# Performance work log

Measured on AMD Instinct MI355X. Metric: run time of the kernel, lower is better.

Reference implementation:

```python
import jax, jax.numpy as jnp
import numpy as np

# ---- dims (match init_kwargs) ----
IMG = 128; PATCH = 16; GRID = IMG // PATCH; L = GRID * GRID  # 64 patches
D = 256            # embed_dim
EXP = 2; DIN = D * EXP          # d_inner = 512
DH = 64; H = DIN // DH          # 8 heads
G = 1; N = 64                   # n_groups, d_state
DCONV = 4
DEPTH = 2
NCLS = 1000
BATCH = 16
DINPROJ = 2 * DIN + 2 * G * N + H   # z | xBC | dt
CDIM = DIN + 2 * G * N              # conv channels
EPS = 1e-6

def _snake_indices():
    g = np.arange(L).reshape(GRID, GRID)
    g[1::2] = g[1::2, ::-1]
    return jnp.asarray(g.reshape(-1))

SNAKE = _snake_indices()

def rmsnorm(x, w):
    return x * jax.lax.rsqrt(jnp.mean(x * x, axis=-1, keepdims=True) + EPS) * w

def causal_depthwise_conv(x, w, b):
    # x: (B,L,C), w: (C,K) depthwise causal conv, then SiLU
    xp = jnp.pad(x, ((0, 0), (DCONV - 1, 0), (0, 0)))
    y = sum(xp[:, k:k + x.shape[1], :] * w[:, k] for k in range(DCONV))
    return jax.nn.silu(y + b)

def mamba_block(x, Win, cw, cb, dtb, Alog, Dp, gn, Wout):
    # Mamba-2/3 style selective scan block. x: (B,L,D)
    Bsz, Lx, _ = x.shape
    zxbcdt = x @ Win                                   # (B,L,DINPROJ)
    z   = zxbcdt[..., :DIN]
    xBC = zxbcdt[..., DIN:DIN + CDIM]
    dt  = jax.nn.softplus(zxbcdt[..., DIN + CDIM:] + dtb)   # (B,L,H)
    xBC = causal_depthwise_conv(xBC, cw, cb)
    xs = xBC[..., :DIN].reshape(Bsz, Lx, H, DH)
    Bm = xBC[..., DIN:DIN + G * N].reshape(Bsz, Lx, G, N)
    Cm = xBC[..., DIN + G * N:].reshape(Bsz, Lx, G, N)
    Bh = jnp.repeat(Bm, H // G, axis=2)                # (B,L,H,N)
    Ch = jnp.repeat(Cm, H // G, axis=2)
    decay = jnp.exp(dt * (-jnp.exp(Alog)))             # (B,L,H) in (0,1)
    dBx = jnp.einsum('blh,blhp,blhn->blhpn', dt, xs, Bh)
    def step(h, inp):
        d, u = inp
        h = d[..., None, None] * h + u
        return h, h
    _, hs = jax.lax.scan(step, jnp.zeros((Bsz, H, DH, N), x.dtype),
                         (jnp.moveaxis(decay, 1, 0), jnp.moveaxis(dBx, 1, 0)))
    hs = jnp.moveaxis(hs, 0, 1)                        # (B,L,H,DH,N)
    y = jnp.einsum('blhpn,blhn->blhp', hs, Ch) + Dp[None, None, :, None] * xs
    y = y.reshape(Bsz, Lx, DIN)
    y = rmsnorm(y * jax.nn.silu(z), gn)                # gated RMSNorm
    return y @ Wout                                    # (B,L,D)

def setup_inputs() -> dict:
    key = jax.random.key(0)
    ks = jax.random.split(key, 24)
    s_in = 1.0 / np.sqrt(D); s_out = 1.0 / np.sqrt(DIN)
    def blk(k):
        kk = jax.random.split(k, 8)
        return dict(
            Win=jax.random.normal(kk[0], (DEPTH, D, DINPROJ)) * s_in,
            cw=jax.random.normal(kk[1], (DEPTH, CDIM, DCONV)) * 0.3,
            cb=jnp.zeros((DEPTH, CDIM)),
            dtb=jax.random.normal(kk[2], (DEPTH, H)) * 0.1,
            Alog=jnp.log(jax.random.uniform(kk[3], (DEPTH, H), minval=1.0, maxval=16.0)),
            Dp=jnp.ones((DEPTH, H)),
            gn=jnp.ones((DEPTH, DIN)),
            Wout=jax.random.normal(kk[4], (DEPTH, DIN, D)) * s_out)
    f = blk(ks[0]); b = blk(ks[1])
    inp = {
        'x': jax.random.normal(ks[2], (BATCH, 3, IMG, IMG), dtype=jnp.float32),
        'patch_w': jax.random.normal(ks[3], (D, 3 * PATCH * PATCH)) * (1.0 / np.sqrt(3 * PATCH * PATCH)),
        'patch_b': jnp.zeros((D,)),
        'pos_embed': jax.random.normal(ks[4], (1, L, D)) * 0.02,
        'norms_w': jnp.ones((DEPTH, D)),
        'final_w': jnp.ones((D,)),
        'head_w': jax.random.normal(ks[5], (D, NCLS)) * (1.0 / np.sqrt(D)),
        'head_b': jnp.zeros((NCLS,)),
    }
    for nm, v in f.items():
        inp[nm + '_f'] = v
    for nm, v in b.items():
        inp[nm + '_b'] = v
    return inp

def reference(x, patch_w, patch_b, pos_embed, norms_w, final_w, head_w, head_b,
              Win_f, cw_f, cb_f, dtb_f, Alog_f, Dp_f, gn_f, Wout_f,
              Win_b, cw_b, cb_b, dtb_b, Alog_b, Dp_b, gn_b, Wout_b):
    Bsz = x.shape[0]
    # patch embed == Conv2d(kernel=stride=PATCH)
    p = x.reshape(Bsz, 3, GRID, PATCH, GRID, PATCH).transpose(0, 2, 4, 1, 3, 5)
    p = p.reshape(Bsz, L, 3 * PATCH * PATCH)
    t = p @ patch_w.T + patch_b                        # (B,L,D)
    t = t + pos_embed[0]
    t = t[:, SNAKE, :]                                 # snake scan order
    for i in range(DEPTH):
        nx = rmsnorm(t, norms_w[i])
        of = mamba_block(nx, Win_f[i], cw_f[i], cb_f[i], dtb_f[i], Alog_f[i], Dp_f[i], gn_f[i], Wout_f[i])
        ob = mamba_block(nx[:, ::-1, :], Win_b[i], cw_b[i], cb_b[i], dtb_b[i], Alog_b[i], Dp_b[i], gn_b[i], Wout_b[i])[:, ::-1, :]
        t = t + 0.5 * (of + ob)                        # drop_path_rate=0 -> identity
    t = rmsnorm(t, final_w)
    t = t.mean(axis=1)
    return t @ head_w + head_b
```

## Files before the change

### kernel.cpp

```cpp
#include <hip/hip_runtime.h>
#include <hip/hip_bf16.h>
#include <math.h>

#define IMG 128
#define PATCH 16
#define L 64
#define D 256
#define DIN 512
#define DH 64
#define H 8
#define NSTATE 64
#define DCONV 4
#define DEPTH 2
#define NCLS 1000
#define BATCH 16
#define DINPROJ 1160
#define CDIM 640
#define EPS 1e-6f

typedef __attribute__((ext_vector_type(8))) short short8;
typedef __attribute__((ext_vector_type(4))) float f32x4;
typedef __attribute__((ext_vector_type(4))) unsigned short us4;
typedef unsigned short ushort_t;

__device__ __forceinline__ int snake_tok(int s){
    int r = s >> 3, c = s & 7;
    return (r & 1) ? (r * 8 + (7 - c)) : (r * 8 + c);
}
__device__ __forceinline__ float silu_f(float x){ return x / (1.f + expf(-x)); }
__device__ __forceinline__ float softplus_f(float x){ return x > 20.f ? x : log1pf(expf(x)); }
__device__ __forceinline__ ushort_t f2b(float f){
    __hip_bfloat16 h = __float2bfloat16(f);
    return *(ushort_t*)&h;
}

__global__ __launch_bounds__(256) void wconv_patch_k(
    const float* __restrict__ Win0, const float* __restrict__ Win1,
    const float* __restrict__ Wout0, const float* __restrict__ Wout1,
    ushort_t* __restrict__ wbuf,
    const float* __restrict__ x, const float* __restrict__ PW,
    float* __restrict__ part)
{
    __shared__ float sm[32][33];
    __shared__ __align__(16) ushort_t As[2][64][40];
    __shared__ __align__(16) ushort_t Bs[2][64][40];
    const int zall = blockIdx.z;
    if (zall < 8){
        int z = zall;
        int R, C; const float* src; ushort_t* dst;
        if (z < 4){
            int layer = z >> 1, dir = z & 1;
            src = (dir ? Win1 : Win0) + (size_t)layer * D * DINPROJ;
            dst = wbuf + (size_t)z * 296960;
            R = D; C = DINPROJ;
        } else {
            int zz = z - 4, layer = zz >> 1, dir = zz & 1;
            src = (dir ? Wout1 : Wout0) + (size_t)layer * DIN * D;
            dst = wbuf + 1187840 + (size_t)zz * 131072;
            R = DIN; C = D;
        }
        int ctiles = (C + 31) >> 5, rtiles = R >> 5;
        if (blockIdx.x >= ctiles || blockIdx.y >= rtiles) return;
        int c0 = blockIdx.x * 32, r0 = blockIdx.y * 32;
        int tx = threadIdx.x & 31, ty = threadIdx.x >> 5;
        #pragma unroll
        for (int k = 0; k < 4; ++k){
            int r = r0 + ty + 8 * k, c = c0 + tx;
            sm[ty + 8 * k][tx] = (c < C) ? src[(size_t)r * C + c] : 0.f;
        }
        __syncthreads();
        #pragma unroll
        for (int k = 0; k < 4; ++k){
            int dr = c0 + ty + 8 * k, dc = r0 + tx;
            if (dr < C) dst[(size_t)dr * R + dc] = f2b(sm[tx][ty + 8 * k]);
        }
        return;
    }
    if (blockIdx.x >= 4) return;
    const int t = threadIdx.x;
    const int n0 = blockIdx.x * 64;
    const int b  = blockIdx.y;
    const int split = zall - 8;
    const int kbase = split * 96;
    const int lrow = t >> 2, lc8 = (t & 3) * 8;
    const int tok = snake_tok(lrow), gy = tok >> 3, gx = tok & 7;
    const float* xb = x + (size_t)b * 3 * IMG * IMG;
    const int wave = t >> 6, lane = t & 63;
    const int wm = (wave >> 1) * 32, wn = (wave & 1) * 32;
    const int fro = lane & 15, fk = (lane >> 4) * 8;

    f32x4 acc[2][2];
    #pragma unroll
    for (int i = 0; i < 2; ++i)
        #pragma unroll
        for (int j = 0; j < 2; ++j) acc[i][j] = (f32x4){0.f,0.f,0.f,0.f};

    short8 areg, breg;
    auto gload = [&](int kk){
        int k = kk + lc8;
        int c = k >> 8, rem = k & 255, py = rem >> 4, px = rem & 15;
        const float* srcA = xb + ((size_t)c * IMG + gy * PATCH + py) * IMG + gx * PATCH + px;
        float4 a0 = *(const float4*)(srcA);
        float4 a1 = *(const float4*)(srcA + 4);
        ushort_t ta[8] = {f2b(a0.x),f2b(a0.y),f2b(a0.z),f2b(a0.w),
                          f2b(a1.x),f2b(a1.y),f2b(a1.z),f2b(a1.w)};
        areg = *(short8*)ta;
        const float* srcB = PW + (size_t)(n0 + lrow) * 768 + kk + lc8;
        float4 b0 = *(const float4*)(srcB);
        float4 b1 = *(const float4*)(srcB + 4);
        ushort_t tb[8] = {f2b(b0.x),f2b(b0.y),f2b(b0.z),f2b(b0.w),
                          f2b(b1.x),f2b(b1.y),f2b(b1.z),f2b(b1.w)};
        breg = *(short8*)tb;
    };
    auto sstore = [&](int buf){
        *(short8*)&As[buf][lrow][lc8] = areg;
        *(short8*)&Bs[buf][lrow][lc8] = breg;
    };

    const int nk = 3;
    gload(kbase); sstore(0);
    __syncthreads();
    for (int kt = 0; kt < nk; ++kt){
        const int buf = kt & 1;
        if (kt + 1 < nk) gload(kbase + (kt + 1) * 32);
        short8 af[2], bfr[2];
        af[0]  = *(const short8*)&As[buf][wm + fro][fk];
        af[1]  = *(const short8*)&As[buf][wm + 16 + fro][fk];
        bfr[0] = *(const short8*)&Bs[buf][wn + fro][fk];
        bfr[1] = *(const short8*)&Bs[buf][wn + 16 + fro][fk];
        #pragma unroll
        for (int i = 0; i < 2; ++i)
            #pragma unroll
            for (int j = 0; j < 2; ++j)
                acc[i][j] = __builtin_amdgcn_mfma_f32_16x16x32_bf16(af[i], bfr[j], acc[i][j], 0, 0, 0);
        if (kt + 1 < nk) sstore(buf ^ 1);
        __syncthreads();
    }
    float* Cp = part + (size_t)split * (BATCH * L * D);
    #pragma unroll
    for (int i = 0; i < 2; ++i){
        #pragma unroll
        for (int j = 0; j < 2; ++j){
            int col = n0 + wn + j * 16 + (lane & 15);
            #pragma unroll
            for (int r = 0; r < 4; ++r){
                int srow = wm + i * 16 + (lane >> 4) * 4 + r;
                Cp[(size_t)(b * 64 + srow) * D + col] = acc[i][j][r];
            }
        }
    }
}

__global__ void patch_red_k(const float* __restrict__ part, const float* __restrict__ pb,
                            const float* __restrict__ pos, float* __restrict__ t){
    int i = blockIdx.x * 256 + threadIdx.x;
    int d = i & (D - 1), s = (i >> 8) & (L - 1);
    float v = 0.f;
    #pragma unroll
    for (int r = 0; r < 8; ++r) v += part[i + r * (BATCH * L * D)];
    t[i] = v + pb[d] + pos[snake_tok(s) * D + d];
}

__global__ __launch_bounds__(256) void gemm_in_k(
    const float* __restrict__ T, const float* __restrict__ nw,
    const ushort_t* __restrict__ B0, const ushort_t* __restrict__ B1,
    const float* __restrict__ cw0, const float* __restrict__ cw1,
    const float* __restrict__ cb0, const float* __restrict__ cb1,
    const float* __restrict__ dtb0, const float* __restrict__ dtb1,
    const float* __restrict__ Al0, const float* __restrict__ Al1,
    float* __restrict__ zb0, float* __restrict__ zb1,
    float* __restrict__ xy0, float* __restrict__ xy1,
    float* __restrict__ bc0, float* __restrict__ bc1,
    float* __restrict__ dts0, float* __restrict__ dts1,
    float* __restrict__ cums0, float* __restrict__ cums1)
{
    __shared__ __align__(16) ushort_t As[64][264];
    __shared__ __align__(16) ushort_t Bs[2][64][40];
    __shared__ float Ctile[64][68];
    const int dir = blockIdx.z;
    const ushort_t* __restrict__ Bw = dir ? B1 : B0;
    const int t = threadIdx.x;
    const int m0 = blockIdx.y * 64, n0 = blockIdx.x * 64;
    const int b = blockIdx.y;
    const int arow = t >> 2;
    const int wave = t >> 6, lane = t & 63;
    const int wm = (wave >> 1) * 32, wn = (wave & 1) * 32;
    const int fro = lane & 15, fk = (lane >> 4) * 8;

    {
        const float* src = T + (size_t)(m0 + arow) * D;
        float ss = 0.f;
        #pragma unroll
        for (int i = 0; i < 16; ++i){
            int c = (t & 3) * 4 + i * 16;
            float4 v = *(const float4*)(src + c);
            ss += v.x*v.x + v.y*v.y + v.z*v.z + v.w*v.w;
        }
        ss += __shfl_xor(ss, 1);
        ss += __shfl_xor(ss, 2);
        float sc = rsqrtf(ss * (1.f / (float)D) + EPS);
        #pragma unroll
        for (int i = 0; i < 16; ++i){
            int c = (t & 3) * 4 + i * 16;
            float4 v = *(const float4*)(src + c);
            float4 w = *(const float4*)(nw + c);
            us4 o = {f2b(v.x*sc*w.x), f2b(v.y*sc*w.y), f2b(v.z*sc*w.z), f2b(v.w*sc*w.w)};
            *(us4*)&As[arow][c] = o;
        }
    }
    const int lrow = t >> 2, lc8 = (t & 3) * 8;
    float4 breg;
    auto gloadB = [&](int kk){
        int gn = n0 + lrow;
        if (gn < DINPROJ) breg = *(const float4*)(Bw + (size_t)gn * D + kk + lc8);
        else breg = make_float4(0.f,0.f,0.f,0.f);
    };
    auto sstoreB = [&](int buf){ *(float4*)&Bs[buf][lrow][lc8] = breg; };

    f32x4 acc[2][2];
    #pragma unroll
    for (int i = 0; i < 2; ++i)
        #pragma unroll
        for (int j = 0; j < 2; ++j) acc[i][j] = (f32x4){0.f,0.f,0.f,0.f};

    gloadB(0); sstoreB(0);
    __syncthreads();
    const int nk = D / 32;
    for (int kt = 0; kt < nk; ++kt){
        const int buf = kt & 1;
        if (kt + 1 < nk) gloadB((kt + 1) * 32);
        short8 af[2], bfr[2];
        af[0]  = *(const short8*)&As[wm + fro][kt * 32 + fk];
        af[1]  = *(const short8*)&As[wm + 16 + fro][kt * 32 + fk];
        bfr[0] = *(const short8*)&Bs[buf][wn + fro][fk];
        bfr[1] = *(const short8*)&Bs[buf][wn + 16 + fro][fk];
        #pragma unroll
        for (int i = 0; i < 2; ++i)
            #pragma unroll
            for (int j = 0; j < 2; ++j)
                acc[i][j] = __builtin_amdgcn_mfma_f32_16x16x32_bf16(af[i], bfr[j], acc[i][j], 0, 0, 0);
        if (kt + 1 < nk) sstoreB(buf ^ 1);
        __syncthreads();
    }

    if (n0 < DIN){
        float* zb = dir ? zb1 : zb0;
        #pragma unroll
        for (int i = 0; i < 2; ++i){
            #pragma unroll
            for (int j = 0; j < 2; ++j){
                int col = n0 + wn + j * 16 + (lane & 15);
                #pragma unroll
                for (int r = 0; r < 4; ++r){
                    int row = m0 + wm + i * 16 + (lane >> 4) * 4 + r;
                    zb[(size_t)row * DIN + col] = acc[i][j][r];
                }
            }
        }
        return;
    }

    #pragma unroll
    for (int i = 0; i < 2; ++i){
        #pragma unroll
        for (int j = 0; j < 2; ++j){
            int lcol = wn + j * 16 + (lane & 15);
            #pragma unroll
            for (int r = 0; r < 4; ++r){
                int lr = wm + i * 16 + (lane >> 4) * 4 + r;
                Ctile[lr][lcol] = acc[i][j][r];
            }
        }
    }
    __syncthreads();

    if (n0 < 1152){
        const float* cw = dir ? cw1 : cw0;
        const float* cb = dir ? cb1 : cb0;
        float* xy = dir ? xy1 : xy0;
        float* bc = dir ? bc1 : bc0;
        const int c = t & 63;
        const int cc = n0 - DIN + c;
        const float w0 = cw[cc * DCONV + 0], w1 = cw[cc * DCONV + 1];
        const float w2 = cw[cc * DCONV + 2], w3 = cw[cc * DCONV + 3];
        const float bb = cb[cc];
        #pragma unroll
        for (int rep = 0; rep < 16; ++rep){
            int s = (t >> 6) + rep * 4;
            float a = bb;
            {
                int sp = s - 3;
                if (sp >= 0) a += w0 * Ctile[dir ? 63 - sp : sp][c];
                sp = s - 2;
                if (sp >= 0) a += w1 * Ctile[dir ? 63 - sp : sp][c];
                sp = s - 1;
                if (sp >= 0) a += w2 * Ctile[dir ? 63 - sp : sp][c];
                a += w3 * Ctile[dir ? 63 - s : s][c];
            }
            float v = silu_f(a);
            if (cc < DIN) xy[(size_t)(b * 64 + s) * DIN + cc] = v;
            else          bc[(size_t)(b * 64 + s) * 128 + (cc - DIN)] = v;
        }
        return;
    }

    {
        const float* dtb = dir ? dtb1 : dtb0;
        const float* Al  = dir ? Al1  : Al0;
        float* dts  = dir ? dts1  : dts0;
        float* cums = dir ? cums1 : cums0;
        int s = t & 63;
        int l = dir ? (63 - s) : s;
        #pragma unroll
        for (int rep = 0; rep < 2; ++rep){
            int h = (t >> 6) + rep * 4;
            float raw = Ctile[l][h] + dtb[h];
            float dt = softplus_f(raw);
            float val = -expf(Al[h]) * dt;
            #pragma unroll
            for (int o = 1; o < 64; o <<= 1){
                float u = __shfl_up(val, o);
                if (s >= o) val += u;
            }
            dts[(size_t)(b * 64 + s) * H + h]  = dt;
            cums[(size_t)(b * 64 + s) * H + h] = val;
        }
    }
}

__global__ __launch_bounds__(512) void yscan2_k(
    const float* __restrict__ bc0, const float* __restrict__ bc1,
    const float* __restrict__ dts0, const float* __restrict__ dts1,
    const float* __restrict__ cums0, const float* __restrict__ cums1,
    const float* __restrict__ Dp0, const float* __restrict__ Dp1,
    const float* __restrict__ zb0, const float* __restrict__ zb1,
    float* __restrict__ xy0, float* __restrict__ xy1,
    float* __restrict__ ssq0, float* __restrict__ ssq1)
{
    __shared__ float Bc[64][65];
    __shared__ float CX[64][65];
    __shared__ float Am[64][65];
    __shared__ float cumS[64], dtS[64];
    __shared__ float ssqp[8][64];
    const int h = blockIdx.x, b = blockIdx.y, dir = blockIdx.z;
    const float* bc   = dir ? bc1   : bc0;
    const float* dts  = dir ? dts1  : dts0;
    const float* cums = dir ? cums1 : cums0;
    const float* Dp   = dir ? Dp1   : Dp0;
    const float* zb   = dir ? zb1   : zb0;
    float* xy  = dir ? xy1  : xy0;
    float* ssq = dir ? ssq1 : ssq0;
    const int t = threadIdx.x;

    if (t < 64){
        cumS[t] = cums[(size_t)(b * L + t) * H + h];
        dtS[t]  = dts[(size_t)(b * L + t) * H + h];
    }
    for (int i = t; i < 4096; i += 512){
        int s = i >> 6, n = i & 63;
        Bc[s][n] = bc[(size_t)(b * L + s) * 128 + n];
        CX[s][n] = bc[(size_t)(b * L + s) * 128 + 64 + n];
    }
    __syncthreads();
    for (int i = t; i < 4096; i += 512){
        int s = i >> 6, j = i & 63;
        float v = 0.f;
        if (j <= s){
            float acc = 0.f;
            #pragma unroll
            for (int n = 0; n < 64; ++n) acc += CX[s][n] * Bc[j][n];
            v = acc * expf(cumS[s] - cumS[j]) * dtS[j];
        }
        Am[s][j] = v;
    }
    __syncthreads();
    for (int i = t; i < 4096; i += 512){
        int j = i >> 6, p = i & 63;
        CX[j][p] = xy[(size_t)(b * L + j) * DIN + h * DH + p];
    }
    __syncthreads();
    {
        const int s = t & 63, pg = t >> 6;
        const int l = dir ? (63 - s) : s;
        const size_t row = (size_t)(b * 64 + l);
        const float dp = Dp[h];
        float acc[8];
        #pragma unroll
        for (int pp = 0; pp < 8; ++pp) acc[pp] = dp * CX[s][pg * 8 + pp];
        #pragma unroll
        for (int j = 0; j < 64; ++j){
            float am = Am[s][j];
            #pragma unroll
            for (int pp = 0; pp < 8; ++pp)
                acc[pp] = fmaf(am, CX[j][pg * 8 + pp], acc[pp]);
        }
        const float* zr = zb + row * DIN + h * DH + pg * 8;
        float4 z0 = *(const float4*)(zr);
        float4 z1 = *(const float4*)(zr + 4);
        float zv[8] = {z0.x, z0.y, z0.z, z0.w, z1.x, z1.y, z1.z, z1.w};
        float g2 = 0.f;
        float gout[8];
        #pragma unroll
        for (int pp = 0; pp < 8; ++pp){
            float g = acc[pp] * silu_f(zv[pp]);
            gout[pp] = g;
            g2 += g * g;
        }
        ssqp[pg][s] = g2;
        float* dst = xy + row * DIN + h * DH + pg * 8;
        *(float4*)(dst)     = make_float4(gout[0], gout[1], gout[2], gout[3]);
        *(float4*)(dst + 4) = make_float4(gout[4], gout[5], gout[6], gout[7]);
    }
    __syncthreads();
    if (t < 64){
        int ll = dir ? (63 - t) : t;
        float v = 0.f;
        #pragma unroll
        for (int q = 0; q < 8; ++q) v += ssqp[q][t];
        ssq[(size_t)(b * 64 + ll) * H + h] = v;
    }
}

__global__ __launch_bounds__(256) void gemm_out_k(
    const float* __restrict__ G0, const float* __restrict__ G1,
    const float* __restrict__ ssq0, const float* __restrict__ ssq1,
    const float* __restrict__ gn0, const float* __restrict__ gn1,
    const ushort_t* __restrict__ B0, const ushort_t* __restrict__ B1,
    float* __restrict__ part)
{
    __shared__ __align__(16) ushort_t As[2][64][40];
    __shared__ __align__(16) ushort_t Bs[2][64][40];
    __shared__ float scl[64];
    const int t = threadIdx.x;
    const int n0 = blockIdx.x * 64, m0 = blockIdx.y * 64;
    const int z = blockIdx.z;
    const int dir = z >> 2;
    const int kbase = (z & 3) * 128;
    const float* __restrict__ G   = dir ? G1   : G0;
    const float* __restrict__ ssq = dir ? ssq1 : ssq0;
    const float* __restrict__ gnw = dir ? gn1  : gn0;
    const ushort_t* __restrict__ B = dir ? B1 : B0;
    const int lrow = t >> 2, lc8 = (t & 3) * 8;
    const int wave = t >> 6, lane = t & 63;
    const int wm = (wave >> 1) * 32, wn = (wave & 1) * 32;
    const int fro = lane & 15, fk = (lane >> 4) * 8;

    if (t < 64){
        const float* sr = ssq + (size_t)(m0 + t) * H;
        float v = (sr[0] + sr[1]) + (sr[2] + sr[3]) + (sr[4] + sr[5]) + (sr[6] + sr[7]);
        scl[t] = rsqrtf(v * (1.f / (float)DIN) + EPS);
    }
    __syncthreads();

    short8 areg; float4 breg;
    auto gload = [&](int kk){
        const float* src = G + (size_t)(m0 + lrow) * DIN + kk + lc8;
        float4 a0 = *(const float4*)(src);
        float4 a1 = *(const float4*)(src + 4);
        const float* gw = gnw + kk + lc8;
        float4 w0 = *(const float4*)(gw);
        float4 w1 = *(const float4*)(gw + 4);
        float sc = scl[lrow];
        ushort_t ta[8] = {f2b(a0.x*sc*w0.x), f2b(a0.y*sc*w0.y), f2b(a0.z*sc*w0.z), f2b(a0.w*sc*w0.w),
                          f2b(a1.x*sc*w1.x), f2b(a1.y*sc*w1.y), f2b(a1.z*sc*w1.z), f2b(a1.w*sc*w1.w)};
        areg = *(short8*)ta;
        breg = *(const float4*)(B + (size_t)(n0 + lrow) * DIN + kk + lc8);
    };
    auto sstore = [&](int buf){
        *(short8*)&As[buf][lrow][lc8] = areg;
        *(float4*)&Bs[buf][lrow][lc8] = breg;
    };

    f32x4 acc[2][2];
    #pragma unroll
    for (int i = 0; i < 2; ++i)
        #pragma unroll
        for (int j = 0; j < 2; ++j) acc[i][j] = (f32x4){0.f,0.f,0.f,0.f};

    const int nk = 4;
    gload(kbase); sstore(0);
    __syncthreads();
    for (int kt = 0; kt < nk; ++kt){
        const int buf = kt & 1;
        if (kt + 1 < nk) gload(kbase + (kt + 1) * 32);
        short8 af[2], bfr[2];
        af[0]  = *(const short8*)&As[buf][wm + fro][fk];
        af[1]  = *(const short8*)&As[buf][wm + 16 + fro][fk];
        bfr[0] = *(const short8*)&Bs[buf][wn + fro][fk];
        bfr[1] = *(const short8*)&Bs[buf][wn + 16 + fro][fk];
        #pragma unroll
        for (int i = 0; i < 2; ++i)
            #pragma unroll
            for (int j = 0; j < 2; ++j)
                acc[i][j] = __builtin_amdgcn_mfma_f32_16x16x32_bf16(af[i], bfr[j], acc[i][j], 0, 0, 0);
        if (kt + 1 < nk) sstore(buf ^ 1);
        __syncthreads();
    }
    float* Cp = part + (size_t)z * (BATCH * L * D);
    #pragma unroll
    for (int i = 0; i < 2; ++i){
        #pragma unroll
        for (int j = 0; j < 2; ++j){
            int col = n0 + wn + j * 16 + (lane & 15);
            #pragma unroll
            for (int r = 0; r < 4; ++r){
                int row = m0 + wm + i * 16 + (lane >> 4) * 4 + r;
                Cp[(size_t)row * D + col] = acc[i][j][r];
            }
        }
    }
}

__global__ void out_red_k(const float* __restrict__ part, float* __restrict__ t){
    int i = blockIdx.x * 256 + threadIdx.x;
    float v = 0.f;
    #pragma unroll
    for (int r = 0; r < 8; ++r) v += part[i + r * (BATCH * L * D)];
    t[i] += 0.5f * v;
}

__global__ void finalmean_k(const float* __restrict__ T, const float* __restrict__ part,
                            const float* __restrict__ fw, float* __restrict__ tm8){
    __shared__ float sm[4];
    int b = blockIdx.x, q = blockIdx.y;
    int d = threadIdx.x;
    float a = 0.f;
    for (int r = 0; r < 8; ++r){
        int row = b * 64 + q * 8 + r;
        size_t o = (size_t)row * D + d;
        float pv = 0.f;
        #pragma unroll
        for (int u = 0; u < 8; ++u) pv += part[o + (size_t)u * (BATCH * L * D)];
        float v = T[o] + 0.5f * pv;
        float ssl = v * v;
        #pragma unroll
        for (int off = 32; off > 0; off >>= 1) ssl += __shfl_down(ssl, off);
        if ((threadIdx.x & 63) == 0) sm[threadIdx.x >> 6] = ssl;
        __syncthreads();
        float ss = sm[0] + sm[1] + sm[2] + sm[3];
        __syncthreads();
        float sc = rsqrtf(ss / (float)D + EPS);
        a += v * sc;
    }
    tm8[(q * BATCH + b) * D + d] = a * (1.f / (float)L) * fw[d];
}

__global__ void head_k(const float* __restrict__ tm8, const float* __restrict__ hw,
                       const float* __restrict__ hb, float* __restrict__ out){
    __shared__ float trs[2][256];
    int i0 = blockIdx.x * 256;
    int mmin = i0 / NCLS;
    int t = threadIdx.x;
    #pragma unroll
    for (int mm = 0; mm < 2; ++mm){
        int m = mmin + mm;
        float v = 0.f;
        if (m < BATCH){
            #pragma unroll
            for (int q = 0; q < 8; ++q)
                v += tm8[(q * BATCH + m) * D + t];
        }
        trs[mm][t] = v;
    }
    __syncthreads();
    int i = i0 + t;
    if (i >= BATCH * NCLS) return;
    int m = i / NCLS, n = i - m * NCLS;
    const float* tr = trs[m - mmin];
    const float* hc = hw + n;
    float a0 = 0.f, a1 = 0.f, a2 = 0.f, a3 = 0.f;
    #pragma unroll 4
    for (int k = 0; k < D; k += 4){
        a0 = fmaf(tr[k],     hc[(size_t)k * NCLS],       a0);
        a1 = fmaf(tr[k + 1], hc[(size_t)(k + 1) * NCLS], a1);
        a2 = fmaf(tr[k + 2], hc[(size_t)(k + 2) * NCLS], a2);
        a3 = fmaf(tr[k + 3], hc[(size_t)(k + 3) * NCLS], a3);
    }
    out[i] = (a0 + a1) + (a2 + a3) + hb[n];
}

extern "C" void kernel_launch(void* const* d_in, const int* in_sizes, int n_in,
                              void* d_out, int out_size, void* d_ws, size_t ws_size,
                              hipStream_t stream){
    (void)in_sizes; (void)n_in; (void)out_size; (void)ws_size;
    const float* x       = (const float*)d_in[0];
    const float* patch_w = (const float*)d_in[1];
    const float* patch_b = (const float*)d_in[2];
    const float* pos     = (const float*)d_in[3];
    const float* norms_w = (const float*)d_in[4];
    const float* final_w = (const float*)d_in[5];
    const float* head_w  = (const float*)d_in[6];
    const float* head_b  = (const float*)d_in[7];
    const float* Win[2]  = {(const float*)d_in[8],  (const float*)d_in[16]};
    const float* cw[2]   = {(const float*)d_in[9],  (const float*)d_in[17]};
    const float* cb[2]   = {(const float*)d_in[10], (const float*)d_in[18]};
    const float* dtb[2]  = {(const float*)d_in[11], (const float*)d_in[19]};
    const float* Alog[2] = {(const float*)d_in[12], (const float*)d_in[20]};
    const float* Dp[2]   = {(const float*)d_in[13], (const float*)d_in[21]};
    const float* gn[2]   = {(const float*)d_in[14], (const float*)d_in[22]};
    const float* Wout[2] = {(const float*)d_in[15], (const float*)d_in[23]};

    float* ws = (float*)d_ws;
    float* t     = ws;
    float* tm8   = t     + 262144;
    float* zb0   = tm8   + 32768;
    float* zb1   = zb0   + 524288;
    float* xy0   = zb1   + 524288;
    float* xy1   = xy0   + 524288;
    float* bc0   = xy1   + 524288;
    float* bc1   = bc0   + 131072;
    float* dts0  = bc1   + 131072;
    float* dts1  = dts0  + 8192;
    float* cum0  = dts1  + 8192;
    float* cum1  = cum0  + 8192;
    float* ssq0  = cum1  + 8192;
    float* ssq1  = ssq0  + 8192;
    float* partP = ssq1  + 8192;
    float* partO = partP + 2097152;
    float* f32end = partO + 2097152;

    ushort_t* wbuf = (ushort_t*)f32end;
    ushort_t* win_bf  = wbuf;
    ushort_t* wout_bf = wbuf + 1187840;

    const int BL = BATCH * L;

    wconv_patch_k<<<dim3(37, 16, 16), 256, 0, stream>>>(
        Win[0], Win[1], Wout[0], Wout[1], wbuf, x, patch_w, partP);
    patch_red_k<<<BL, 256, 0, stream>>>(partP, patch_b, pos, t);

    for (int i = 0; i < DEPTH; ++i){
        const float* cw0  = cw[0]   + (size_t)i * CDIM * DCONV;
        const float* cw1  = cw[1]   + (size_t)i * CDIM * DCONV;
        const float* cb0  = cb[0]   + (size_t)i * CDIM;
        const float* cb1  = cb[1]   + (size_t)i * CDIM;
        const float* dtb0 = dtb[0]  + (size_t)i * H;
        const float* dtb1 = dtb[1]  + (size_t)i * H;
        const float* Al0  = Alog[0] + (size_t)i * H;
        const float* Al1  = Alog[1] + (size_t)i * H;
        const float* Dp0  = Dp[0]   + (size_t)i * H;
        const float* Dp1  = Dp[1]   + (size_t)i * H;
        const float* gn0  = gn[0]   + (size_t)i * DIN;
        const float* gn1  = gn[1]   + (size_t)i * DIN;
        const ushort_t* Wi0 = win_bf  + (size_t)(2 * i + 0) * 296960;
        const ushort_t* Wi1 = win_bf  + (size_t)(2 * i + 1) * 296960;
        const ushort_t* Wo0 = wout_bf + (size_t)(2 * i + 0) * 131072;
        const ushort_t* Wo1 = wout_bf + (size_t)(2 * i + 1) * 131072;

        gemm_in_k<<<dim3(19, 16, 2), 256, 0, stream>>>(
            t, norms_w + i * D, Wi0, Wi1, cw0, cw1, cb0, cb1, dtb0, dtb1,
            Al0, Al1, zb0, zb1, xy0, xy1, bc0, bc1, dts0, dts1, cum0, cum1);
        yscan2_k<<<dim3(H, BATCH, 2), 512, 0, stream>>>(
            bc0, bc1, dts0, dts1, cum0, cum1, Dp0, Dp1, zb0, zb1,
            xy0, xy1, ssq0, ssq1);
        gemm_out_k<<<dim3(4, 16, 8), 256, 0, stream>>>(
            xy0, xy1, ssq0, ssq1, gn0, gn1, Wo0, Wo1, partO);
        if (i == 0)
            out_red_k<<<BL, 256, 0, stream>>>(partO, t);
    }

    finalmean_k<<<dim3(BATCH, 8), 256, 0, stream>>>(t, partO, final_w, tm8);
    head_k<<<(BATCH * NCLS + 255) / 256, 256, 0, stream>>>(
        tm8, head_w, head_b, (float*)d_out);
}
```

Before: 130.9 us.

## Fold split-K reductions into consumer kernels and drop residual buffer

Removes the patch_red_k and out_red_k launches. The partial sums from the patch-embed and out-projection GEMMs are now reduced inside gemm_in_k and finalmean_k, which recompute the residual stream from partials plus bias and positional embedding. Split-K factors are reduced (patch 8→2, out 8→4 per direction), so fewer partial slabs are written and read, and the weight-transpose/patch kernel uses a flat 1D task grid with no idle blocks. The cost is fewer, longer blocks in those GEMMs and redundant partial loads in every gemm_in_k column block.

```diff
diff --git a/kernel.cpp b/kernel.cpp
--- a/kernel.cpp
+++ b/kernel.cpp
@@ -17,6 +17,7 @@
 #define DINPROJ 1160
 #define CDIM 640
 #define EPS 1e-6f
+#define SLAB (BATCH * L * D)
 
 typedef __attribute__((ext_vector_type(8))) short short8;
 typedef __attribute__((ext_vector_type(4))) float f32x4;
@@ -39,30 +40,29 @@
     const float* __restrict__ Wout0, const float* __restrict__ Wout1,
     ushort_t* __restrict__ wbuf,
     const float* __restrict__ x, const float* __restrict__ PW,
-    float* __restrict__ part)
+    float* __restrict__ partP)
 {
-    __shared__ float sm[32][33];
-    __shared__ __align__(16) ushort_t As[2][64][40];
-    __shared__ __align__(16) ushort_t Bs[2][64][40];
-    const int zall = blockIdx.z;
-    if (zall < 8){
-        int z = zall;
-        int R, C; const float* src; ushort_t* dst;
-        if (z < 4){
-            int layer = z >> 1, dir = z & 1;
-            src = (dir ? Win1 : Win0) + (size_t)layer * D * DINPROJ;
+    __shared__ __align__(16) unsigned char SM[20480];
+    const int task = blockIdx.x;
+    const int tid = threadIdx.x;
+    if (task < 1696){
+        float (*sm)[33] = (float(*)[33])SM;
+        const float* src; ushort_t* dst; int R, C, ctiles, tile;
+        if (task < 1184){
+            int z = task / 296; tile = task - z * 296;
+            src = (z & 1 ? Win1 : Win0) + (size_t)(z >> 1) * D * DINPROJ;
             dst = wbuf + (size_t)z * 296960;
-            R = D; C = DINPROJ;
+            R = D; C = DINPROJ; ctiles = 37;
         } else {
-            int zz = z - 4, layer = zz >> 1, dir = zz & 1;
-            src = (dir ? Wout1 : Wout0) + (size_t)layer * DIN * D;
-            dst = wbuf + 1187840 + (size_t)zz * 131072;
-            R = DIN; C = D;
-        }
-        int ctiles = (C + 31) >> 5, rtiles = R >> 5;
-        if (blockIdx.x >= ctiles || blockIdx.y >= rtiles) return;
-        int c0 = blockIdx.x * 32, r0 = blockIdx.y * 32;
-        int tx = threadIdx.x & 31, ty = threadIdx.x >> 5;
+            int k = task - 1184;
+            int z = k >> 7; tile = k & 127;
+            src = (z & 1 ? Wout1 : Wout0) + (size_t)(z >> 1) * DIN * D;
+            dst = wbuf + 1187840 + (size_t)z * 131072;
+            R = DIN; C = D; ctiles = 8;
+        }
+        int cx = tile % ctiles, ry = tile / ctiles;
+        int c0 = cx * 32, r0 = ry * 32;
+        int tx = tid & 31, ty = tid >> 5;
         #pragma unroll
         for (int k = 0; k < 4; ++k){
             int r = r0 + ty + 8 * k, c = c0 + tx;
@@ -76,16 +76,16 @@
         }
         return;
     }
-    if (blockIdx.x >= 4) return;
-    const int t = threadIdx.x;
-    const int n0 = blockIdx.x * 64;
-    const int b  = blockIdx.y;
-    const int split = zall - 8;
-    const int kbase = split * 96;
-    const int lrow = t >> 2, lc8 = (t & 3) * 8;
+    ushort_t (*As)[64][40] = (ushort_t(*)[64][40])SM;
+    ushort_t (*Bs)[64][40] = (ushort_t(*)[64][40])(SM + 10240);
+    const int pt = task - 1696;
+    const int xi = pt & 3, b = (pt >> 2) & 15, split = pt >> 6;
+    const int n0 = xi * 64;
+    const int kbase = split * 384;
+    const int lrow = tid >> 2, lc8 = (tid & 3) * 8;
     const int tok = snake_tok(lrow), gy = tok >> 3, gx = tok & 7;
     const float* xb = x + (size_t)b * 3 * IMG * IMG;
-    const int wave = t >> 6, lane = t & 63;
+    const int wave = tid >> 6, lane = tid & 63;
     const int wm = (wave >> 1) * 32, wn = (wave & 1) * 32;
     const int fro = lane & 15, fk = (lane >> 4) * 8;
 
@@ -117,7 +117,7 @@
         *(short8*)&Bs[buf][lrow][lc8] = breg;
     };
 
-    const int nk = 3;
+    const int nk = 12;
     gload(kbase); sstore(0);
     __syncthreads();
     for (int kt = 0; kt < nk; ++kt){
@@ -136,7 +136,7 @@
         if (kt + 1 < nk) sstore(buf ^ 1);
         __syncthreads();
     }
-    float* Cp = part + (size_t)split * (BATCH * L * D);
+    float* Cp = partP + (size_t)split * SLAB;
     #pragma unroll
     for (int i = 0; i < 2; ++i){
         #pragma unroll
@@ -151,18 +151,10 @@
     }
 }
 
-__global__ void patch_red_k(const float* __restrict__ part, const float* __restrict__ pb,
-                            const float* __restrict__ pos, float* __restrict__ t){
-    int i = blockIdx.x * 256 + threadIdx.x;
-    int d = i & (D - 1), s = (i >> 8) & (L - 1);
-    float v = 0.f;
-    #pragma unroll
-    for (int r = 0; r < 8; ++r) v += part[i + r * (BATCH * L * D)];
-    t[i] = v + pb[d] + pos[snake_tok(s) * D + d];
-}
-
 __global__ __launch_bounds__(256) void gemm_in_k(
-    const float* __restrict__ T, const float* __restrict__ nw,
+    const float* __restrict__ partP, const float* __restrict__ pb,
+    const float* __restrict__ pos, const float* __restrict__ pO,
+    const float* __restrict__ nw,
     const ushort_t* __restrict__ B0, const ushort_t* __restrict__ B1,
     const float* __restrict__ cw0, const float* __restrict__ cw1,
     const float* __restrict__ cb0, const float* __restrict__ cb1,
@@ -179,21 +171,43 @@
     __shared__ float Ctile[64][68];
     const int dir = blockIdx.z;
     const ushort_t* __restrict__ Bw = dir ? B1 : B0;
-    const int t = threadIdx.x;
+    const int tid = threadIdx.x;
     const int m0 = blockIdx.y * 64, n0 = blockIdx.x * 64;
     const int b = blockIdx.y;
-    const int arow = t >> 2;
-    const int wave = t >> 6, lane = t & 63;
+    const int arow = tid >> 2;
+    const int wave = tid >> 6, lane = tid & 63;
     const int wm = (wave >> 1) * 32, wn = (wave & 1) * 32;
     const int fro = lane & 15, fk = (lane >> 4) * 8;
 
     {
-        const float* src = T + (size_t)(m0 + arow) * D;
+        const int row = m0 + arow;
+        const int tokr = snake_tok(row & 63);
+        float4 vr[16];
         float ss = 0.f;
         #pragma unroll
         for (int i = 0; i < 16; ++i){
-            int c = (t & 3) * 4 + i * 16;
-            float4 v = *(const float4*)(src + c);
+            int c = (tid & 3) * 4 + i * 16;
+            size_t o = (size_t)row * D + c;
+            float4 p0 = *(const float4*)(partP + o);
+            float4 p1 = *(const float4*)(partP + SLAB + o);
+            float4 bb = *(const float4*)(pb + c);
+            float4 ps = *(const float4*)(pos + (size_t)tokr * D + c);
+            float4 v;
+            v.x = p0.x + p1.x + bb.x + ps.x;
+            v.y = p0.y + p1.y + bb.y + ps.y;
+            v.z = p0.z + p1.z + bb.z + ps.z;
+            v.w = p0.w + p1.w + bb.w + ps.w;
+            if (pO){
+                float4 o0 = *(const float4*)(pO + o);
+                float4 o1 = *(const float4*)(pO + SLAB + o);
+                float4 o2 = *(const float4*)(pO + 2 * SLAB + o);
+                float4 o3 = *(const float4*)(pO + 3 * SLAB + o);
+                v.x += 0.5f * ((o0.x + o1.x) + (o2.x + o3.x));
+                v.y += 0.5f * ((o0.y + o1.y) + (o2.y + o3.y));
+                v.z += 0.5f * ((o0.z + o1.z) + (o2.z + o3.z));
+                v.w += 0.5f * ((o0.w + o1.w) + (o2.w + o3.w));
+            }
+            vr[i] = v;
             ss += v.x*v.x + v.y*v.y + v.z*v.z + v.w*v.w;
         }
         ss += __shfl_xor(ss, 1);
@@ -201,14 +215,14 @@
         float sc = rsqrtf(ss * (1.f / (float)D) + EPS);
         #pragma unroll
         for (int i = 0; i < 16; ++i){
-            int c = (t & 3) * 4 + i * 16;
-            float4 v = *(const float4*)(src + c);
+            int c = (tid & 3) * 4 + i * 16;
             float4 w = *(const float4*)(nw + c);
-            us4 o = {f2b(v.x*sc*w.x), f2b(v.y*sc*w.y), f2b(v.z*sc*w.z), f2b(v.w*sc*w.w)};
-            *(us4*)&As[arow][c] = o;
-        }
-    }
-    const int lrow = t >> 2, lc8 = (t & 3) * 8;
+            float4 v = vr[i];
+            us4 ov = {f2b(v.x*sc*w.x), f2b(v.y*sc*w.y), f2b(v.z*sc*w.z), f2b(v.w*sc*w.w)};
+            *(us4*)&As[arow][c] = ov;
+        }
+    }
+    const int lrow = tid >> 2, lc8 = (tid & 3) * 8;
     float4 breg;
     auto gloadB = [&](int kk){
         int gn = n0 + lrow;
@@ -274,19 +288,19 @@
     }
     __syncthreads();
 
-    if (n0 < 1152){
+    if (blockIdx.x < 18){
         const float* cw = dir ? cw1 : cw0;
         const float* cb = dir ? cb1 : cb0;
         float* xy = dir ? xy1 : xy0;
         float* bc = dir ? bc1 : bc0;
-        const int c = t & 63;
+        const int c = tid & 63;
         const int cc = n0 - DIN + c;
         const float w0 = cw[cc * DCONV + 0], w1 = cw[cc * DCONV + 1];
         const float w2 = cw[cc * DCONV + 2], w3 = cw[cc * DCONV + 3];
         const float bb = cb[cc];
         #pragma unroll
         for (int rep = 0; rep < 16; ++rep){
-            int s = (t >> 6) + rep * 4;
+            int s = (tid >> 6) + rep * 4;
             float a = bb;
             {
                 int sp = s - 3;
@@ -309,11 +323,11 @@
         const float* Al  = dir ? Al1  : Al0;
         float* dts  = dir ? dts1  : dts0;
         float* cums = dir ? cums1 : cums0;
-        int s = t & 63;
+        int s = tid & 63;
         int l = dir ? (63 - s) : s;
         #pragma unroll
         for (int rep = 0; rep < 2; ++rep){
-            int h = (t >> 6) + rep * 4;
+            int h = (tid >> 6) + rep * 4;
             float raw = Ctile[l][h] + dtb[h];
             float dt = softplus_f(raw);
             float val = -expf(Al[h]) * dt;
@@ -375,8 +389,8 @@
     }
     __syncthreads();
     for (int i = t; i < 4096; i += 512){
-        int j = i >> 6, p = i & 63;
-        CX[j][p] = xy[(size_t)(b * L + j) * DIN + h * DH + p];
+        int j = i >> 6, pp = i & 63;
+        CX[j][pp] = xy[(size_t)(b * L + j) * DIN + h * DH + pp];
     }
     __syncthreads();
     {
@@ -431,24 +445,24 @@
     __shared__ __align__(16) ushort_t As[2][64][40];
     __shared__ __align__(16) ushort_t Bs[2][64][40];
     __shared__ float scl[64];
-    const int t = threadIdx.x;
+    const int tid = threadIdx.x;
     const int n0 = blockIdx.x * 64, m0 = blockIdx.y * 64;
     const int z = blockIdx.z;
-    const int dir = z >> 2;
-    const int kbase = (z & 3) * 128;
+    const int dir = z >> 1;
+    const int kbase = (z & 1) * 256;
     const float* __restrict__ G   = dir ? G1   : G0;
     const float* __restrict__ ssq = dir ? ssq1 : ssq0;
     const float* __restrict__ gnw = dir ? gn1  : gn0;
     const ushort_t* __restrict__ B = dir ? B1 : B0;
-    const int lrow = t >> 2, lc8 = (t & 3) * 8;
-    const int wave = t >> 6, lane = t & 63;
+    const int lrow = tid >> 2, lc8 = (tid & 3) * 8;
+    const int wave = tid >> 6, lane = tid & 63;
     const int wm = (wave >> 1) * 32, wn = (wave & 1) * 32;
     const int fro = lane & 15, fk = (lane >> 4) * 8;
 
-    if (t < 64){
-        const float* sr = ssq + (size_t)(m0 + t) * H;
+    if (tid < 64){
+        const float* sr = ssq + (size_t)(m0 + tid) * H;
         float v = (sr[0] + sr[1]) + (sr[2] + sr[3]) + (sr[4] + sr[5]) + (sr[6] + sr[7]);
-        scl[t] = rsqrtf(v * (1.f / (float)DIN) + EPS);
+        scl[tid] = rsqrtf(v * (1.f / (float)DIN) + EPS);
     }
     __syncthreads();
 
@@ -477,7 +491,7 @@
         #pragma unroll
         for (int j = 0; j < 2; ++j) acc[i][j] = (f32x4){0.f,0.f,0.f,0.f};
 
-    const int nk = 4;
+    const int nk = 8;
     gload(kbase); sstore(0);
     __syncthreads();
     for (int kt = 0; kt < nk; ++kt){
@@ -496,7 +510,7 @@
         if (kt + 1 < nk) sstore(buf ^ 1);
         __syncthreads();
     }
-    float* Cp = part + (size_t)z * (BATCH * L * D);
+    float* Cp = part + (size_t)z * SLAB;
     #pragma unroll
     for (int i = 0; i < 2; ++i){
         #pragma unroll
@@ -511,33 +525,27 @@
     }
 }
 
-__global__ void out_red_k(const float* __restrict__ part, float* __restrict__ t){
-    int i = blockIdx.x * 256 + threadIdx.x;
-    float v = 0.f;
-    #pragma unroll
-    for (int r = 0; r < 8; ++r) v += part[i + r * (BATCH * L * D)];
-    t[i] += 0.5f * v;
-}
-
-__global__ void finalmean_k(const float* __restrict__ T, const float* __restrict__ part,
+__global__ void finalmean_k(const float* __restrict__ partP, const float* __restrict__ pb,
+                            const float* __restrict__ pos,
+                            const float* __restrict__ pO0, const float* __restrict__ pO1,
                             const float* __restrict__ fw, float* __restrict__ tm8){
-    __shared__ float sm[4];
+    __shared__ float sm4[4];
     int b = blockIdx.x, q = blockIdx.y;
     int d = threadIdx.x;
     float a = 0.f;
     for (int r = 0; r < 8; ++r){
         int row = b * 64 + q * 8 + r;
+        int tokr = snake_tok(row & 63);
         size_t o = (size_t)row * D + d;
-        float pv = 0.f;
-        #pragma unroll
-        for (int u = 0; u < 8; ++u) pv += part[o + (size_t)u * (BATCH * L * D)];
-        float v = T[o] + 0.5f * pv;
+        float v = (partP[o] + partP[SLAB + o]) + pb[d] + pos[(size_t)tokr * D + d];
+        v += 0.5f * ((pO0[o] + pO0[SLAB + o]) + (pO0[2 * SLAB + o] + pO0[3 * SLAB + o]));
+        v += 0.5f * ((pO1[o] + pO1[SLAB + o]) + (pO1[2 * SLAB + o] + pO1[3 * SLAB + o]));
         float ssl = v * v;
         #pragma unroll
         for (int off = 32; off > 0; off >>= 1) ssl += __shfl_down(ssl, off);
-        if ((threadIdx.x & 63) == 0) sm[threadIdx.x >> 6] = ssl;
+        if ((threadIdx.x & 63) == 0) sm4[threadIdx.x >> 6] = ssl;
         __syncthreads();
-        float ss = sm[0] + sm[1] + sm[2] + sm[3];
+        float ss = sm4[0] + sm4[1] + sm4[2] + sm4[3];
         __syncthreads();
         float sc = rsqrtf(ss / (float)D + EPS);
         a += v * sc;
@@ -601,8 +609,7 @@
     const float* Wout[2] = {(const float*)d_in[15], (const float*)d_in[23]};
 
     float* ws = (float*)d_ws;
-    float* t     = ws;
-    float* tm8   = t     + 262144;
+    float* tm8   = ws;
     float* zb0   = tm8   + 32768;
     float* zb1   = zb0   + 524288;
     float* xy0   = zb1   + 524288;
@@ -616,19 +623,18 @@
     float* ssq0  = cum1  + 8192;
     float* ssq1  = ssq0  + 8192;
     float* partP = ssq1  + 8192;
-    float* partO = partP + 2097152;
-    float* f32end = partO + 2097152;
+    float* partO0= partP + 524288;
+    float* partO1= partO0+ 1048576;
+    float* f32end = partO1 + 1048576;
 
     ushort_t* wbuf = (ushort_t*)f32end;
     ushort_t* win_bf  = wbuf;
     ushort_t* wout_bf = wbuf + 1187840;
 
-    const int BL = BATCH * L;
-
-    wconv_patch_k<<<dim3(37, 16, 16), 256, 0, stream>>>(
+    wconv_patch_k<<<1824, 256, 0, stream>>>(
         Win[0], Win[1], Wout[0], Wout[1], wbuf, x, patch_w, partP);
-    patch_red_k<<<BL, 256, 0, stream>>>(partP, patch_b, pos, t);
-
+
+    float* partOs[2] = {partO0, partO1};
     for (int i = 0; i < DEPTH; ++i){
         const float* cw0  = cw[0]   + (size_t)i * CDIM * DCONV;
         const float* cw1  = cw[1]   + (size_t)i * CDIM * DCONV;
@@ -646,20 +652,21 @@
         const ushort_t* Wi1 = win_bf  + (size_t)(2 * i + 1) * 296960;
         const ushort_t* Wo0 = wout_bf + (size_t)(2 * i + 0) * 131072;
         const ushort_t* Wo1 = wout_bf + (size_t)(2 * i + 1) * 131072;
+        const float* pO = (i == 0) ? nullptr : partO0;
 
         gemm_in_k<<<dim3(19, 16, 2), 256, 0, stream>>>(
-            t, norms_w + i * D, Wi0, Wi1, cw0, cw1, cb0, cb1, dtb0, dtb1,
-            Al0, Al1, zb0, zb1, xy0, xy1, bc0, bc1, dts0, dts1, cum0, cum1);
+            partP, patch_b, pos, pO, norms_w + i * D, Wi0, Wi1,
+            cw0, cw1, cb0, cb1, dtb0, dtb1, Al0, Al1,
+            zb0, zb1, xy0, xy1, bc0, bc1, dts0, dts1, cum0, cum1);
         yscan2_k<<<dim3(H, BATCH, 2), 512, 0, stream>>>(
             bc0, bc1, dts0, dts1, cum0, cum1, Dp0, Dp1, zb0, zb1,
             xy0, xy1, ssq0, ssq1);
-        gemm_out_k<<<dim3(4, 16, 8), 256, 0, stream>>>(
-            xy0, xy1, ssq0, ssq1, gn0, gn1, Wo0, Wo1, partO);
-        if (i == 0)
-            out_red_k<<<BL, 256, 0, stream>>>(partO, t);
-    }
-
-    finalmean_k<<<dim3(BATCH, 8), 256, 0, stream>>>(t, partO, final_w, tm8);
+        gemm_out_k<<<dim3(4, 16, 4), 256, 0, stream>>>(
+            xy0, xy1, ssq0, ssq1, gn0, gn1, Wo0, Wo1, partOs[i]);
+    }
+
+    finalmean_k<<<dim3(BATCH, 8), 256, 0, stream>>>(
+        partP, patch_b, pos, partO0, partO1, final_w, tm8);
     head_k<<<(BATCH * NCLS + 255) / 256, 256, 0, stream>>>(
         tm8, head_w, head_b, (float*)d_out);
 }
```

New measurement: 140.6 us. +7.4%, slower.
